# Optimization experiments

Hardware: AMD Instinct MI355X
Metric: run time of the kernel (lower is better)

## Reference

```python
import jax, jax.numpy as jnp
import numpy as np

N = 4096
PED_SPEED = 1.34   # desired pedestrian speed (m/s)
K = 2.0            # goal-attraction gain
ALPHA = 10.66      # repulsion strength
PED_RADIUS = 0.3
PED_MASS = 60.0
BETTA = 0.71       # repulsion range
DT = 0.4
COST_A = 1.0       # goal-progress weight
COST_B = 1.0       # blame (proximity) weight
COST_E = 1.0       # blame length scale
EPS = 1e-8


def calc_forces(state, goals):
    pos = state[:, 0:2]            # [N,2]
    vel = state[:, 2:4]            # [N,2]
    # O(N^2) pairwise social repulsion
    delta = pos[:, None, :] - pos[None, :, :]                    # [N,N,2]
    dist = jnp.sqrt(jnp.sum(delta * delta, axis=-1) + EPS)       # [N,N]
    mag = ALPHA * jnp.exp((2.0 * PED_RADIUS - dist) / BETTA)     # [N,N]
    mag = mag * (1.0 - jnp.eye(pos.shape[0], dtype=pos.dtype))   # zero self-force
    rep_force = jnp.sum((mag / dist)[..., None] * delta, axis=1)  # [N,2]
    # attraction toward goal: relax velocity to desired velocity
    to_goal = goals - pos
    gd = jnp.sqrt(jnp.sum(to_goal * to_goal, axis=-1, keepdims=True) + EPS)
    attr_force = K * PED_MASS * (PED_SPEED * to_goal / gd - vel)
    return rep_force, attr_force


def pose_propagation(F, state):
    pos = state[:, 0:2]
    vel = state[:, 2:4]
    vel_new = vel + (F / PED_MASS) * DT
    speed = jnp.sqrt(jnp.sum(vel_new * vel_new, axis=-1, keepdims=True) + EPS)
    vel_new = vel_new * jnp.minimum(1.0, PED_SPEED / speed)  # clamp to max speed
    pos_new = pos + vel_new * DT
    return jnp.concatenate([pos_new, vel_new], axis=1)      # [N,4]


def calc_cost_function(goals, robot_init_pose, state, observed_state):
    pos = state[:, 0:2]
    robot_pose = pos[0]  # agent 0 is the robot
    goal_vec = goals[0] - robot_init_pose
    pg = jnp.dot(pos[0] - robot_init_pose, goal_vec) / (jnp.sqrt(jnp.sum(goal_vec * goal_vec)) + EPS)
    dist_rp = jnp.sqrt(jnp.sum((pos - robot_pose) ** 2, axis=-1) + EPS)  # [N]
    blame = COST_B * jnp.exp(-dist_rp / COST_E)
    dev = jnp.sum((pos - observed_state[:, 0:2]) ** 2, axis=-1)
    return -COST_A * pg + blame + dev  # [N]


def setup_inputs():
    key = jax.random.key(0)
    k1, k2, k3, k4 = jax.random.split(key, 4)
    scale = jnp.array([10.0, 10.0, 1.0, 1.0], dtype=jnp.float32)
    state = jax.random.normal(k1, (N, 4), dtype=jnp.float32) * scale
    goals = jax.random.normal(k2, (N, 2), dtype=jnp.float32) * 10.0
    robot_init_pose = jax.random.normal(k3, (2,), dtype=jnp.float32) * 10.0
    observed_state = jax.random.normal(k4, (N, 4), dtype=jnp.float32) * scale
    cost = jnp.zeros((N, 1), dtype=jnp.float32)
    return {"state": state, "cost": cost, "goals": goals,
            "robot_init_pose": robot_init_pose, "observed_state": observed_state}


def reference(state, cost, goals, robot_init_pose, observed_state):
    rf, af = calc_forces(state, goals)
    F = rf + af
    out = pose_propagation(F, state)
    temp = calc_cost_function(goals, robot_init_pose, out, observed_state)
    cost_new = cost + temp.reshape(-1, 1)
    return out, cost_new
```

## Files before the change

### kernel.cpp

```cpp
#include <hip/hip_runtime.h>

#define N 4096
#define EPS 1e-8f

__global__ __launch_bounds__(256) void rep_pairs(const float4* __restrict__ state4,
                                                 float2* __restrict__ part) {
    __shared__ float2 sj[32];
    const int tid = threadIdx.x;
    const int jb  = blockIdx.y;
    const int i   = blockIdx.x * 256 + tid;

    if (tid < 32) {
        const float4 s = state4[jb * 32 + tid];
        sj[tid] = make_float2(s.x, s.y);
    }
    const float4 si = state4[i];
    const float xi = si.x, yi = si.y;
    __syncthreads();

    const float C1 = 1.44269504088896340736f / 0.71f;
    const float C0 = 0.6f * C1 + 3.41414351f;

    float fx0 = 0.f, fy0 = 0.f, fx1 = 0.f, fy1 = 0.f;
#pragma unroll 4
    for (int jj = 0; jj < 32; jj += 2) {
        {
            const float2 pj = sj[jj];
            const float dx   = xi - pj.x;
            const float dy   = yi - pj.y;
            const float r2   = fmaf(dx, dx, fmaf(dy, dy, EPS));
            const float inv  = __builtin_amdgcn_rsqf(r2);
            const float d    = r2 * inv;
            const float coef = __builtin_amdgcn_exp2f(fmaf(d, -C1, C0)) * inv;
            fx0 = fmaf(coef, dx, fx0);
            fy0 = fmaf(coef, dy, fy0);
        }
        {
            const float2 pj = sj[jj + 1];
            const float dx   = xi - pj.x;
            const float dy   = yi - pj.y;
            const float r2   = fmaf(dx, dx, fmaf(dy, dy, EPS));
            const float inv  = __builtin_amdgcn_rsqf(r2);
            const float d    = r2 * inv;
            const float coef = __builtin_amdgcn_exp2f(fmaf(d, -C1, C0)) * inv;
            fx1 = fmaf(coef, dx, fx1);
            fy1 = fmaf(coef, dy, fy1);
        }
    }
    part[(size_t)jb * N + i] = make_float2(fx0 + fx1, fy0 + fy1);
}

__global__ __launch_bounds__(256) void reduce_prop(const float* __restrict__ state,
                                                   const float* __restrict__ goals,
                                                   const float2* __restrict__ part,
                                                   float* __restrict__ out,
                                                   int nbj) {
    __shared__ float2 red[256];
    const int tid = threadIdx.x;
    const int il  = tid & 31;
    const int ks  = tid >> 5;
    const int i   = blockIdx.x * 32 + il;
    const int kper = nbj >> 3;

    float fx = 0.f, fy = 0.f;
    for (int k = ks * kper; k < ks * kper + kper; ++k) {
        const float2 p = part[(size_t)k * N + i];
        fx += p.x; fy += p.y;
    }
    red[tid] = make_float2(fx, fy);
    __syncthreads();

    if (ks == 0) {
#pragma unroll
        for (int s = 1; s < 8; ++s) {
            fx += red[s * 32 + il].x;
            fy += red[s * 32 + il].y;
        }
        const float px = state[i * 4 + 0], py = state[i * 4 + 1];
        const float vx = state[i * 4 + 2], vy = state[i * 4 + 3];
        const float gx = goals[i * 2 + 0] - px, gy = goals[i * 2 + 1] - py;
        const float gd = sqrtf(fmaf(gx, gx, fmaf(gy, gy, EPS)));
        fx += 120.f * (1.34f * gx / gd - vx);
        fy += 120.f * (1.34f * gy / gd - vy);
        float vnx = fmaf(fx, 0.4f / 60.f, vx);
        float vny = fmaf(fy, 0.4f / 60.f, vy);
        const float sp  = sqrtf(fmaf(vnx, vnx, fmaf(vny, vny, EPS)));
        const float fac = fminf(1.f, 1.34f / sp);
        vnx *= fac; vny *= fac;
        out[i * 4 + 0] = fmaf(vnx, 0.4f, px);
        out[i * 4 + 1] = fmaf(vny, 0.4f, py);
        out[i * 4 + 2] = vnx;
        out[i * 4 + 3] = vny;
    }
}

__global__ __launch_bounds__(256) void cost_k(const float* __restrict__ cost_in,
                                              const float* __restrict__ goals,
                                              const float* __restrict__ rip,
                                              const float* __restrict__ obs,
                                              const float* __restrict__ new_state,
                                              float* __restrict__ cost_out) {
    const int i = blockIdx.x * 256 + threadIdx.x;
    const float rx = rip[0], ry = rip[1];
    const float gvx = goals[0] - rx, gvy = goals[1] - ry;
    const float p0x = new_state[0], p0y = new_state[1];
    const float pg = ((p0x - rx) * gvx + (p0y - ry) * gvy)
                   / (sqrtf(gvx * gvx + gvy * gvy) + EPS);
    const float pnx = new_state[i * 4 + 0], pny = new_state[i * 4 + 1];
    const float ddx = pnx - p0x, ddy = pny - p0y;
    const float dist_rp = sqrtf(fmaf(ddx, ddx, fmaf(ddy, ddy, EPS)));
    const float blame = expf(-dist_rp);
    const float ox = obs[i * 4 + 0], oy = obs[i * 4 + 1];
    const float dev = (pnx - ox) * (pnx - ox) + (pny - oy) * (pny - oy);
    cost_out[i] = cost_in[i] + (-pg + blame + dev);
}

extern "C" void kernel_launch(void* const* d_in, const int* in_sizes, int n_in,
                              void* d_out, int out_size, void* d_ws, size_t ws_size,
                              hipStream_t stream) {
    const float* state = (const float*)d_in[0];
    const float* cost  = (const float*)d_in[1];
    const float* goals = (const float*)d_in[2];
    const float* rip   = (const float*)d_in[3];
    const float* obs   = (const float*)d_in[4];
    float* out  = (float*)d_out;
    float2* part = (float2*)d_ws;

    const int nbj = 128;

    rep_pairs<<<dim3(16, nbj), 256, 0, stream>>>((const float4*)state, part);
    reduce_prop<<<N / 32, 256, 0, stream>>>(state, goals, part, out, nbj);
    cost_k<<<N / 256, 256, 0, stream>>>(cost, goals, rip, obs, out, out + 4 * N);
}
```

Baseline: 76.36 us.

## Fuse cost into finalize kernel and halve j-block partials

Each pairwise block now covers 64 j-agents instead of 32, which halves the number of partial force rows written to and read from the workspace and halves the grid to 1024 blocks. The reduction/propagation kernel and the cost kernel are merged into one. Each block redundantly reduces agent 0's partials with a wavefront shuffle so the robot's new position is known without a third launch. The fused kernel uses 32 blocks, so it has low occupancy, and the pairwise kernel has fewer blocks to spread over the CUs.

```diff
diff --git a/kernel.cpp b/kernel.cpp
--- a/kernel.cpp
+++ b/kernel.cpp
@@ -1,17 +1,18 @@
 #include <hip/hip_runtime.h>
 
 #define N 4096
+#define NBJ 64
 #define EPS 1e-8f
 
 __global__ __launch_bounds__(256) void rep_pairs(const float4* __restrict__ state4,
                                                  float2* __restrict__ part) {
-    __shared__ float2 sj[32];
+    __shared__ float2 sj[64];
     const int tid = threadIdx.x;
     const int jb  = blockIdx.y;
     const int i   = blockIdx.x * 256 + tid;
 
-    if (tid < 32) {
-        const float4 s = state4[jb * 32 + tid];
+    if (tid < 64) {
+        const float4 s = state4[jb * 64 + tid];
         sj[tid] = make_float2(s.x, s.y);
     }
     const float4 si = state4[i];
@@ -22,8 +23,8 @@
     const float C0 = 0.6f * C1 + 3.41414351f;
 
     float fx0 = 0.f, fy0 = 0.f, fx1 = 0.f, fy1 = 0.f;
-#pragma unroll 4
-    for (int jj = 0; jj < 32; jj += 2) {
+#pragma unroll 8
+    for (int jj = 0; jj < 64; jj += 2) {
         {
             const float2 pj = sj[jj];
             const float dx   = xi - pj.x;
@@ -50,32 +51,54 @@
     part[(size_t)jb * N + i] = make_float2(fx0 + fx1, fy0 + fy1);
 }
 
-__global__ __launch_bounds__(256) void reduce_prop(const float* __restrict__ state,
-                                                   const float* __restrict__ goals,
-                                                   const float2* __restrict__ part,
-                                                   float* __restrict__ out,
-                                                   int nbj) {
-    __shared__ float2 red[256];
+__global__ __launch_bounds__(256) void finalize(const float* __restrict__ state,
+                                                const float* __restrict__ cost_in,
+                                                const float* __restrict__ goals,
+                                                const float* __restrict__ rip,
+                                                const float4* __restrict__ obs4,
+                                                const float2* __restrict__ part,
+                                                float* __restrict__ out) {
+    __shared__ float2 red[2][128];
+    __shared__ float2 s_p0;
     const int tid = threadIdx.x;
-    const int il  = tid & 31;
-    const int ks  = tid >> 5;
-    const int i   = blockIdx.x * 32 + il;
-    const int kper = nbj >> 3;
+    const int il  = tid & 127;
+    const int ks  = tid >> 7;
+    const int i   = blockIdx.x * 128 + il;
 
     float fx = 0.f, fy = 0.f;
-    for (int k = ks * kper; k < ks * kper + kper; ++k) {
+    for (int k = ks * 32; k < ks * 32 + 32; ++k) {
         const float2 p = part[(size_t)k * N + i];
         fx += p.x; fy += p.y;
     }
-    red[tid] = make_float2(fx, fy);
+    red[ks][il] = make_float2(fx, fy);
+
+    if (tid < 64) {
+        float2 f0 = part[(size_t)tid * N + 0];
+#pragma unroll
+        for (int off = 32; off > 0; off >>= 1) {
+            f0.x += __shfl_down(f0.x, off);
+            f0.y += __shfl_down(f0.y, off);
+        }
+        if (tid == 0) {
+            const float px = state[0], py = state[1], vx = state[2], vy = state[3];
+            const float gx = goals[0] - px, gy = goals[1] - py;
+            const float gd = sqrtf(fmaf(gx, gx, fmaf(gy, gy, EPS)));
+            const float Fx = f0.x + 120.f * (1.34f * gx / gd - vx);
+            const float Fy = f0.y + 120.f * (1.34f * gy / gd - vy);
+            float vnx = fmaf(Fx, 0.4f / 60.f, vx);
+            float vny = fmaf(Fy, 0.4f / 60.f, vy);
+            const float sp  = sqrtf(fmaf(vnx, vnx, fmaf(vny, vny, EPS)));
+            const float fac = fminf(1.f, 1.34f / sp);
+            vnx *= fac; vny *= fac;
+            s_p0 = make_float2(fmaf(vnx, 0.4f, px), fmaf(vny, 0.4f, py));
+        }
+    }
     __syncthreads();
 
     if (ks == 0) {
-#pragma unroll
-        for (int s = 1; s < 8; ++s) {
-            fx += red[s * 32 + il].x;
-            fy += red[s * 32 + il].y;
-        }
+        fx += red[1][il].x;
+        fy += red[1][il].y;
+
         const float px = state[i * 4 + 0], py = state[i * 4 + 1];
         const float vx = state[i * 4 + 2], vy = state[i * 4 + 3];
         const float gx = goals[i * 2 + 0] - px, gy = goals[i * 2 + 1] - py;
@@ -87,32 +110,27 @@
         const float sp  = sqrtf(fmaf(vnx, vnx, fmaf(vny, vny, EPS)));
         const float fac = fminf(1.f, 1.34f / sp);
         vnx *= fac; vny *= fac;
-        out[i * 4 + 0] = fmaf(vnx, 0.4f, px);
-        out[i * 4 + 1] = fmaf(vny, 0.4f, py);
+        const float pnx = fmaf(vnx, 0.4f, px);
+        const float pny = fmaf(vny, 0.4f, py);
+
+        out[i * 4 + 0] = pnx;
+        out[i * 4 + 1] = pny;
         out[i * 4 + 2] = vnx;
         out[i * 4 + 3] = vny;
+
+        const float rx = rip[0], ry = rip[1];
+        const float gvx = goals[0] - rx, gvy = goals[1] - ry;
+        const float p0x = s_p0.x, p0y = s_p0.y;
+        const float pg = ((p0x - rx) * gvx + (p0y - ry) * gvy)
+                       / (sqrtf(gvx * gvx + gvy * gvy) + EPS);
+        const float ddx = pnx - p0x, ddy = pny - p0y;
+        const float dist_rp = sqrtf(fmaf(ddx, ddx, fmaf(ddy, ddy, EPS)));
+        const float blame = __expf(-dist_rp);
+        const float4 ob = obs4[i];
+        const float dev = (pnx - ob.x) * (pnx - ob.x) + (pny - ob.y) * (pny - ob.y);
+
+        out[4 * N + i] = cost_in[i] + (-pg + blame + dev);
     }
-}
-
-__global__ __launch_bounds__(256) void cost_k(const float* __restrict__ cost_in,
-                                              const float* __restrict__ goals,
-                                              const float* __restrict__ rip,
-                                              const float* __restrict__ obs,
-                                              const float* __restrict__ new_state,
-                                              float* __restrict__ cost_out) {
-    const int i = blockIdx.x * 256 + threadIdx.x;
-    const float rx = rip[0], ry = rip[1];
-    const float gvx = goals[0] - rx, gvy = goals[1] - ry;
-    const float p0x = new_state[0], p0y = new_state[1];
-    const float pg = ((p0x - rx) * gvx + (p0y - ry) * gvy)
-                   / (sqrtf(gvx * gvx + gvy * gvy) + EPS);
-    const float pnx = new_state[i * 4 + 0], pny = new_state[i * 4 + 1];
-    const float ddx = pnx - p0x, ddy = pny - p0y;
-    const float dist_rp = sqrtf(fmaf(ddx, ddx, fmaf(ddy, ddy, EPS)));
-    const float blame = expf(-dist_rp);
-    const float ox = obs[i * 4 + 0], oy = obs[i * 4 + 1];
-    const float dev = (pnx - ox) * (pnx - ox) + (pny - oy) * (pny - oy);
-    cost_out[i] = cost_in[i] + (-pg + blame + dev);
 }
 
 extern "C" void kernel_launch(void* const* d_in, const int* in_sizes, int n_in,
@@ -123,12 +141,11 @@
     const float* goals = (const float*)d_in[2];
     const float* rip   = (const float*)d_in[3];
     const float* obs   = (const float*)d_in[4];
-    float* out  = (float*)d_out;
+    float* out   = (float*)d_out;
     float2* part = (float2*)d_ws;
 
-    const int nbj = 128;
-
-    rep_pairs<<<dim3(16, nbj), 256, 0, stream>>>((const float4*)state, part);
-    reduce_prop<<<N / 32, 256, 0, stream>>>(state, goals, part, out, nbj);
-    cost_k<<<N / 256, 256, 0, stream>>>(cost, goals, rip, obs, out, out + 4 * N);
+    rep_pairs<<<dim3(16, NBJ), 256, 0, stream>>>((const float4*)state, part);
+    finalize<<<N / 128, 256, 0, stream>>>(state, cost, goals, rip,
+                                          (const float4*)state == nullptr ? nullptr : (const float4*)d_in[4],
+                                          part, out);
 }
```

Measured after the change: 70.33 us. -7.9%, faster.
